# Performance work log

Hardware: AMD Instinct MI355X
Metric: run time of the kernel (lower is better)

The kernel has to match this reference:

```python
import jax, jax.numpy as jnp
import numpy as np

N, M, E = 100000, 500, 300000
XS, GS, OUT, HEADS = 100, 100, 100, 2
SLOPE = 0.2
EPS = 1e-12


def l2norm(x, axis):
    n = jnp.linalg.norm(x, axis=axis, keepdims=True)
    return x / jnp.maximum(n, EPS)


def gat_layer(h_ijk, ends, n, W, att):
    # W: [heads*out, in_dim] (no bias); att: [1, heads, out]
    heads, out = att.shape[1], att.shape[2]
    c = (h_ijk @ W.T).reshape(-1, heads, out)               # [E, H, D]
    a = jnp.sum(att * c, axis=2, keepdims=True)             # [E, H, 1]
    e = jnp.exp(-jax.nn.leaky_relu(a, SLOPE))
    denom = jax.ops.segment_sum(e, ends, num_segments=n)    # [n, H, 1]
    alpha = e / denom[ends]                                 # segment softmax (dropout=eval/identity)
    h = jax.ops.segment_sum(alpha * c, ends, num_segments=n)  # [n, H, D]
    h = jax.nn.elu(h)
    h = l2norm(h, axis=2)
    return h.reshape(n, heads * out)


def merge_layer(h_in, h_out, Wi, bi, Wo, bo, Wl, bl):
    hi = h_in @ Wi.T + bi
    ho = h_out @ Wo.T + bo
    lam = jax.nn.sigmoid(jnp.concatenate([hi, ho], axis=1) @ Wl.T + bl)
    h = lam * hi + (1.0 - lam) * ho
    return l2norm(jax.nn.elu(h), axis=1)


def setup_inputs() -> dict:
    key = jax.random.key(0)
    ks = jax.random.split(key, 24)
    D = HEADS * OUT  # 200
    in1 = 2 * XS + GS   # 300
    in2 = 3 * D         # 600
    s = 0.05
    return {
        'edge_idx': jax.random.randint(ks[0], (2, E), 0, N),
        'edge_type': jax.random.randint(ks[1], (E,), 0, M),
        'path_idx': jax.random.randint(ks[2], (2, 8), 0, N),
        'path_type': jax.random.randint(ks[3], (2, 8), 0, M),
        'use_path': 0,
        'x': jax.random.normal(ks[4], (N, XS), jnp.float32),
        'g': jax.random.normal(ks[5], (M, GS), jnp.float32),
        'W_in1': s * jax.random.normal(ks[6], (D, in1), jnp.float32),
        'att_in1': s * jax.random.normal(ks[7], (1, HEADS, OUT), jnp.float32),
        'W_out1': s * jax.random.normal(ks[8], (D, in1), jnp.float32),
        'att_out1': s * jax.random.normal(ks[9], (1, HEADS, OUT), jnp.float32),
        'Wi1': s * jax.random.normal(ks[10], (D, D), jnp.float32), 'bi1': jnp.zeros((D,), jnp.float32),
        'Wo1': s * jax.random.normal(ks[11], (D, D), jnp.float32), 'bo1': jnp.zeros((D,), jnp.float32),
        'Wl1': s * jax.random.normal(ks[12], (1, 2 * D), jnp.float32), 'bl1': jnp.zeros((1,), jnp.float32),
        'Wr': s * jax.random.normal(ks[13], (D, GS), jnp.float32), 'br': jnp.zeros((D,), jnp.float32),
        'Wf': s * jax.random.normal(ks[14], (D, in1), jnp.float32), 'bf': jnp.zeros((D,), jnp.float32),
        'W_in2': s * jax.random.normal(ks[15], (D, in2), jnp.float32),
        'att_in2': s * jax.random.normal(ks[16], (1, 1, D), jnp.float32),
        'W_out2': s * jax.random.normal(ks[17], (D, in2), jnp.float32),
        'att_out2': s * jax.random.normal(ks[18], (1, 1, D), jnp.float32),
        'Wi2': s * jax.random.normal(ks[19], (D, D), jnp.float32), 'bi2': jnp.zeros((D,), jnp.float32),
        'Wo2': s * jax.random.normal(ks[20], (D, D), jnp.float32), 'bo2': jnp.zeros((D,), jnp.float32),
        'Wl2': s * jax.random.normal(ks[21], (1, 2 * D), jnp.float32), 'bl2': jnp.zeros((1,), jnp.float32),
        'W_ent': s * jax.random.normal(ks[22], (D, XS), jnp.float32),
    }


def reference(edge_idx, edge_type, path_idx, path_type, use_path, x, g,
              W_in1, att_in1, W_out1, att_out1, Wi1, bi1, Wo1, bo1, Wl1, bl1,
              Wr, br, Wf, bf,
              W_in2, att_in2, W_out2, att_out2, Wi2, bi2, Wo2, bo2, Wl2, bl2,
              W_ent):
    n, m = x.shape[0], g.shape[0]
    x = l2norm(x, axis=1)  # x_initial is renormalized each forward
    row, col = edge_idx[0], edge_idx[1]
    # hop 1: gather-concat per-edge features [E, 2*XS+GS]
    h_ijk = jnp.concatenate([x[row], x[col], g[edge_type]], axis=1)
    h_in = gat_layer(h_ijk, col, n, W_in1, att_in1)
    h_out = gat_layer(h_ijk, row, n, W_out1, att_out1)
    h = merge_layer(h_in, h_out, Wi1, bi1, Wo1, bo1, Wl1, bl1)
    # relation layer
    g_edges = jax.ops.segment_sum(h_ijk, edge_type, num_segments=m)
    g_edges = jax.nn.elu(l2norm(g_edges, axis=1))
    g_prime = (g @ Wr.T + br) + (g_edges @ Wf.T + bf)
    # hop 2
    h_ijk2 = jnp.concatenate([h[row], h[col], g_prime[edge_type]], axis=1)
    h_in2 = gat_layer(h_ijk2, col, n, W_in2, att_in2)
    h_out2 = gat_layer(h_ijk2, row, n, W_out2, att_out2)
    h = merge_layer(h_in2, h_out2, Wi2, bi2, Wo2, bo2, Wl2, bl2)
    # entity residual layer
    h_prime = x @ W_ent.T + h
    return h_prime
```

## Files before the change

### kernel.cpp

```cpp
#include <hip/hip_runtime.h>
#include <cstddef>
#include <cstdint>

#define WSLOPE 0.2f
#define WEPS 1e-12f

typedef __attribute__((ext_vector_type(8))) short bf16x8;
typedef __attribute__((ext_vector_type(4))) float f32x4;

__device__ __forceinline__ float waveSum(float v) {
#pragma unroll
    for (int off = 32; off > 0; off >>= 1) v += __shfl_xor(v, off, 64);
    return v;
}
__device__ __forceinline__ float eluf(float v) { return v > 0.f ? v : expm1f(v); }
__device__ __forceinline__ short f2bf(float f) {
    union { float f; uint32_t u; } v; v.f = f;
    uint32_t r = v.u + 0x7FFF + ((v.u >> 16) & 1);
    return (short)(r >> 16);
}

__global__ void k_invnorm(const float* __restrict__ x, float* __restrict__ invn, int N) {
    int wid = blockIdx.x * 4 + (threadIdx.x >> 6);
    int lane = threadIdx.x & 63;
    if (wid >= N) return;
    const float* p = x + (size_t)wid * 100;
    float a = p[lane];
    float ss = a * a;
    if (lane < 36) { float b = p[lane + 64]; ss += b * b; }
    ss = waveSum(ss);
    if (lane == 0) invn[wid] = 1.f / fmaxf(sqrtf(ss), WEPS);
}

__global__ void k_count(const int* __restrict__ keys, int* __restrict__ cnt, int n) {
    int i = blockIdx.x * 256 + threadIdx.x;
    if (i < n) atomicAdd(&cnt[keys[i]], 1);
}

#define SCAN_CHUNK 2048
__global__ void k_blocksum(const int* __restrict__ cnt, int* __restrict__ bsum, int n) {
    __shared__ int sh[256];
    int b = blockIdx.x, t = threadIdx.x;
    int base = b * SCAN_CHUNK;
    int s = 0;
    for (int i = t; i < SCAN_CHUNK; i += 256) { int idx = base + i; if (idx < n) s += cnt[idx]; }
    sh[t] = s; __syncthreads();
    for (int off = 128; off > 0; off >>= 1) { if (t < off) sh[t] += sh[t + off]; __syncthreads(); }
    if (t == 0) bsum[b] = sh[0];
}

__global__ void k_scanwrite(const int* __restrict__ cnt, const int* __restrict__ bsum,
                            int* __restrict__ offs, int* __restrict__ cur, int n, int nb) {
    __shared__ int sh[256];
    __shared__ int sbase;
    int b = blockIdx.x, t = threadIdx.x;
    if (t == 0) { int s = 0; for (int i = 0; i < b; ++i) s += bsum[i]; sbase = s; }
    __syncthreads();
    int base = b * SCAN_CHUNK;
    int loc[8]; int ts = 0;
#pragma unroll
    for (int i = 0; i < 8; ++i) { int idx = base + t * 8 + i; int v = (idx < n) ? cnt[idx] : 0; loc[i] = ts; ts += v; }
    sh[t] = ts; __syncthreads();
    for (int off = 1; off < 256; off <<= 1) {
        int v = (t >= off) ? sh[t - off] : 0;
        __syncthreads();
        sh[t] += v;
        __syncthreads();
    }
    int excl = (t == 0) ? 0 : sh[t - 1];
    int gbase = sbase + excl;
#pragma unroll
    for (int i = 0; i < 8; ++i) {
        int idx = base + t * 8 + i;
        if (idx < n) { offs[idx] = gbase + loc[i]; cur[idx] = gbase + loc[i]; }
    }
    if (b == nb - 1 && t == 255) offs[n] = sbase + sh[255];
}

__global__ void k_scatter(const int* __restrict__ keys, int* __restrict__ cur, int* __restrict__ lists, int n) {
    int i = blockIdx.x * 256 + threadIdx.x;
    if (i < n) { int p = atomicAdd(&cur[keys[i]], 1); lists[p] = i; }
}

__global__ void k_watt(const float* __restrict__ att, const float* __restrict__ W,
                       float* __restrict__ wa, int H, int DH, int K) {
    int id = blockIdx.x * 256 + threadIdx.x;
    if (id >= H * K) return;
    int h = id / K, k = id % K;
    float s = 0.f;
    for (int j = 0; j < DH; ++j) s += att[h * DH + j] * W[(size_t)(h * DH + j) * K + k];
    wa[id] = s;
}

template<bool HOP2>
__global__ void k_dots(const float* __restrict__ feat, const float* __restrict__ invn,
                       const float* __restrict__ wa, float* __restrict__ rdot,
                       float* __restrict__ cdot, int N) {
    int wid = blockIdx.x * 4 + (threadIdx.x >> 6);
    int lane = threadIdx.x & 63;
    if (wid >= N) return;
    if (!HOP2) {
        float inv = invn[wid];
        const float* p = feat + (size_t)wid * 100;
        float f0 = p[lane] * inv;
        float f1 = (lane < 36) ? p[lane + 64] * inv : 0.f;
#pragma unroll
        for (int h = 0; h < 2; ++h) {
            const float* w = wa + h * 300;
            float r = f0 * w[lane] + ((lane < 36) ? f1 * w[lane + 64] : 0.f);
            float c = f0 * w[100 + lane] + ((lane < 36) ? f1 * w[100 + lane + 64] : 0.f);
            r = waveSum(r); c = waveSum(c);
            if (lane == 0) { rdot[wid * 2 + h] = r; cdot[wid * 2 + h] = c; }
        }
    } else {
        const float* p = feat + (size_t)wid * 200;
        float r = 0.f, c = 0.f;
#pragma unroll
        for (int m = 0; m < 4; ++m) {
            int d = lane + m * 64;
            if (d < 200) { float f = p[d]; r += f * wa[d]; c += f * wa[200 + d]; }
        }
        r = waveSum(r); c = waveSum(c);
        if (lane == 0) { rdot[wid] = r; cdot[wid] = c; }
    }
}

__global__ void k_gdot(const float* __restrict__ gsrc, const float* __restrict__ wa,
                       float* __restrict__ gdot, int M, int H, int GL, int K) {
    int id = blockIdx.x * 256 + threadIdx.x;
    if (id >= M * H) return;
    int m = id / H, h = id % H;
    float s = 0.f;
    const float* w = wa + h * K + 2 * GL;
    const float* gm = gsrc + (size_t)m * GL;
    for (int kk = 0; kk < GL; ++kk) s += gm[kk] * w[kk];
    gdot[id] = s;
}

__global__ void k_projg(const float* __restrict__ gsrc, const float* __restrict__ W,
                        float* __restrict__ pg, int M, int GL, int K) {
    int id = blockIdx.x * 256 + threadIdx.x;
    if (id >= M * 200) return;
    int m = id / 200, d = id % 200;
    float s = 0.f;
    const float* gm = gsrc + (size_t)m * GL;
    const float* w = W + (size_t)d * K + 2 * GL;
    for (int kk = 0; kk < GL; ++kk) s += gm[kk] * w[kk];
    pg[id] = s;
}

__global__ void k_ew(const int* __restrict__ row, const int* __restrict__ col, const int* __restrict__ et,
                     const float* __restrict__ rdot, const float* __restrict__ cdot,
                     const float* __restrict__ gdot, float* __restrict__ ew, int E, int H) {
    int id = blockIdx.x * 256 + threadIdx.x;
    if (id >= E * H) return;
    int e = id / H, h = id - e * H;
    float a = rdot[row[e] * H + h] + cdot[col[e] * H + h] + gdot[et[e] * H + h];
    float lr = a > 0.f ? a : WSLOPE * a;
    ew[id] = expf(-lr);
}

template<int H, bool HOP2>
__global__ void k_agg(const int* __restrict__ offs, const int* __restrict__ lists,
                      const int* __restrict__ nbrArr, const int* __restrict__ etype,
                      const float* __restrict__ ew, const float* __restrict__ projg,
                      const float* __restrict__ feat, const float* __restrict__ invn,
                      short* __restrict__ agg_b, float* __restrict__ hb, int n0, int n1) {
    int node = n0 + blockIdx.x * 4 + (threadIdx.x >> 6);
    int lane = threadIdx.x & 63;
    if (node >= n1) return;
    int o = offs[node];
    int deg = offs[node + 1] - o;
    float va[7];
#pragma unroll
    for (int m = 0; m < 7; ++m) va[m] = 0.f;
    if (deg > 0) {
        float s0 = 0.f, s1 = 0.f;
        for (int i = lane; i < deg; i += 64) {
            int e = lists[o + i];
            s0 += ew[e * H];
            if (H == 2) s1 += ew[e * H + 1];
        }
        s0 = waveSum(s0);
        float rd0 = 1.f / s0, rd1 = rd0;
        if (H == 2) { s1 = waveSum(s1); rd1 = 1.f / s1; }
        for (int j = 0; j < deg; ++j) {
            int e = lists[o + j];
            float a0 = ew[e * H] * rd0;
            float a1 = (H == 2) ? ew[e * H + 1] * rd1 : a0;
            int nbr = nbrArr[e];
            int et = etype[e];
            const float* pgr = projg + (size_t)et * 200;
            if (!HOP2) {
                float inv = invn[nbr];
                const float* fr = feat + (size_t)nbr * 100;
#pragma unroll
                for (int m = 0; m < 7; ++m) {
                    int d = lane + m * 64;
                    if (d < 200) {
                        int kk = d >= 100 ? d - 100 : d;
                        float al = d < 100 ? a0 : a1;
                        va[m] += al * fr[kk] * inv;
                    } else if (d < 400) {
                        int dd = d - 200;
                        float al = dd < 100 ? a0 : a1;
                        va[m] += al * pgr[dd];
                    }
                }
            } else {
                const float* fr = feat + (size_t)nbr * 200;
#pragma unroll
                for (int m = 0; m < 7; ++m) {
                    int d = lane + m * 64;
                    if (d < 200) va[m] += a0 * fr[d];
                    else if (d < 400) va[m] += a0 * pgr[d - 200];
                }
            }
        }
    }
    size_t rb = (size_t)(node - n0);
#pragma unroll
    for (int m = 0; m < 7; ++m) {
        int d = lane + m * 64;
        if (d < 200) {
            int slot = HOP2 ? d : (d < 100 ? d : d + 12);
            agg_b[rb * 224 + slot] = f2bf(va[m]);
        } else if (d < 400) {
            hb[rb * 200 + (d - 200)] = va[m];
        }
    }
    if (!HOP2) {
        if (lane < 24) { int s = lane < 12 ? 100 + lane : 200 + lane; agg_b[rb * 224 + s] = 0; }
    } else {
        if (lane < 24) agg_b[rb * 224 + 200 + lane] = 0;
    }
}

template<int KSTEPS, bool BIAS, bool ACC, bool DEGMASK>
__launch_bounds__(256)
__global__ void k_mgemm(const short* __restrict__ A, const short* __restrict__ Wb,
                        const float* __restrict__ bias, const int* __restrict__ degoffs,
                        float* __restrict__ out, int rows) {
    constexpr int LDA = KSTEPS * 32;
    const int t = threadIdx.x;
    const int wv = t >> 6, l = t & 63;
    const int lhi = l >> 4, llo = l & 15;
    const int rbase = blockIdx.x * 64 + wv * 16;
    f32x4 acc[13];
#pragma unroll
    for (int j = 0; j < 13; ++j) acc[j] = f32x4{0.f, 0.f, 0.f, 0.f};
    const short* arow = A + (size_t)(rbase + llo) * LDA + lhi * 8;
#pragma unroll
    for (int kt = 0; kt < KSTEPS; ++kt) {
        bf16x8 a = *(const bf16x8*)(arow + kt * 32);
#pragma unroll
        for (int j = 0; j < 13; ++j) {
            bf16x8 b = *(const bf16x8*)(Wb + (size_t)(j * 16 + llo) * LDA + kt * 32 + lhi * 8);
            acc[j] = __builtin_amdgcn_mfma_f32_16x16x32_bf16(a, b, acc[j], 0, 0, 0);
        }
    }
    const int r0 = rbase + lhi * 4;
#pragma unroll
    for (int e = 0; e < 4; ++e) {
        int r = r0 + e;
        if (r >= rows) continue;
        float dm = 1.f;
        if (DEGMASK) dm = (degoffs[r + 1] - degoffs[r] == 0) ? 0.f : 1.f;
        float* orow = out + (size_t)r * 200;
#pragma unroll
        for (int j = 0; j < 13; ++j) {
            int d = j * 16 + llo;
            if (d < 200) {
                float v = acc[j][e] * dm;
                if (BIAS) v += bias[d];
                if (ACC) v += orow[d];
                orow[d] = v;
            }
        }
    }
}

__global__ void k_prepw(const float* __restrict__ W, int ldW, int koff, int Klen, int Kpad,
                        int mode, short* __restrict__ Wb) {
    int id = blockIdx.x * 256 + threadIdx.x;
    int tot = 208 * Kpad;
    if (id >= tot) return;
    int d = id / Kpad, k = id - d * Kpad;
    float v = 0.f;
    if (d < 200) {
        if (mode == 0) { if (k < Klen) v = W[(size_t)d * ldW + koff + k]; }
        else { int h = d / 100; int kk = k - h * 112; if (kk >= 0 && kk < 100) v = W[(size_t)d * ldW + koff + kk]; }
    }
    Wb[id] = f2bf(v);
}

__global__ void k_xcb(const float* __restrict__ x, const float* __restrict__ invn,
                      short* __restrict__ sb, int rows) {
    int id = blockIdx.x * 256 + threadIdx.x;
    if (id >= rows * 128) return;
    int r = id >> 7, k = id & 127;
    sb[id] = f2bf(k < 100 ? x[(size_t)r * 100 + k] * invn[r] : 0.f);
}

__global__ void k_h1b(const float* __restrict__ h1, short* __restrict__ sb, int rows) {
    int id = blockIdx.x * 256 + threadIdx.x;
    if (id >= rows * 224) return;
    int r = id / 224, k = id - r * 224;
    sb[id] = f2bf(k < 200 ? h1[(size_t)r * 200 + k] : 0.f);
}

template<int DH, int H>
__global__ void gat_post2(const float* __restrict__ hb, short* __restrict__ pb, int rowsH) {
    int nh = blockIdx.x * 4 + (threadIdx.x >> 6);
    int lane = threadIdx.x & 63;
    if (nh >= rowsH) return;
    const float* p = hb + (size_t)nh * DH;
    constexpr int MM = (DH + 63) / 64;
    float v[MM];
    float ss = 0.f;
#pragma unroll
    for (int m = 0; m < MM; ++m) {
        int d = lane + m * 64;
        v[m] = 0.f;
        if (d < DH) { v[m] = eluf(p[d]); ss += v[m] * v[m]; }
    }
    ss = waveSum(ss);
    float inv = 1.f / fmaxf(sqrtf(ss), WEPS);
    short* ob = pb + (size_t)(nh / H) * 224 + (size_t)(nh % H) * DH;
#pragma unroll
    for (int m = 0; m < MM; ++m) {
        int d = lane + m * 64;
        if (d < DH) ob[d] = f2bf(v[m] * inv);
    }
}

__global__ void merge_comb(const float* __restrict__ hi, const float* __restrict__ ho,
                           const float* __restrict__ Wl, const float* __restrict__ bl,
                           float* __restrict__ out, int N) {
    int wid = blockIdx.x * 4 + (threadIdx.x >> 6);
    int lane = threadIdx.x & 63;
    if (wid >= N) return;
    float vi[4], vo[4];
    float s = 0.f;
#pragma unroll
    for (int m = 0; m < 4; ++m) {
        int d = lane + m * 64;
        vi[m] = 0.f; vo[m] = 0.f;
        if (d < 200) {
            vi[m] = hi[(size_t)wid * 200 + d];
            vo[m] = ho[(size_t)wid * 200 + d];
            s += Wl[d] * vi[m] + Wl[200 + d] * vo[m];
        }
    }
    s = waveSum(s);
    float lam = 1.f / (1.f + expf(-(s + bl[0])));
    float hv[4];
    float ss = 0.f;
#pragma unroll
    for (int m = 0; m < 4; ++m) {
        int d = lane + m * 64;
        hv[m] = 0.f;
        if (d < 200) {
            float h = lam * vi[m] + (1.f - lam) * vo[m];
            hv[m] = eluf(h);
            ss += hv[m] * hv[m];
        }
    }
    ss = waveSum(ss);
    float inv = 1.f / fmaxf(sqrtf(ss), WEPS);
#pragma unroll
    for (int m = 0; m < 4; ++m) {
        int d = lane + m * 64;
        if (d < 200) out[(size_t)wid * 200 + d] = hv[m] * inv;
    }
}

__global__ void k_gedges(const int* __restrict__ eidx, const int* __restrict__ lists,
                         const int* __restrict__ offs,
                         const float* __restrict__ x, const float* __restrict__ invn,
                         const float* __restrict__ g, float* __restrict__ ge_n, int E) {
    __shared__ float red[5];
    __shared__ float stot;
    int m = blockIdx.x, t = threadIdx.x;
    int o = offs[m];
    int n = offs[m + 1] - o;
    float acc = 0.f;
    if (t < 200) {
        for (int i = 0; i < n; ++i) {
            int e = lists[o + i];
            if (t < 100) { int r = eidx[e];     acc += x[(size_t)r * 100 + t] * invn[r]; }
            else         { int r = eidx[E + e]; acc += x[(size_t)r * 100 + t - 100] * invn[r]; }
        }
    } else if (t < 300) {
        acc = (float)n * g[(size_t)m * 100 + (t - 200)];
    }
    float sq = (t < 300) ? acc * acc : 0.f;
    sq = waveSum(sq);
    if ((t & 63) == 0) red[t >> 6] = sq;
    __syncthreads();
    if (t == 0) {
        float s2 = 0.f;
        for (int i = 0; i < 5; ++i) s2 += red[i];
        stot = 1.f / fmaxf(sqrtf(s2), WEPS);
    }
    __syncthreads();
    if (t < 300) ge_n[(size_t)m * 300 + t] = eluf(acc * stot);
}

__global__ void k_gprime(const float* __restrict__ g, const float* __restrict__ ge_n,
                         const float* __restrict__ Wr, const float* __restrict__ br,
                         const float* __restrict__ Wf, const float* __restrict__ bf,
                         float* __restrict__ gp, int M) {
    int m = blockIdx.x, d = threadIdx.x;
    if (d >= 200) return;
    float s = br[d] + bf[d];
    const float* gm = g + (size_t)m * 100;
    const float* gem = ge_n + (size_t)m * 300;
    const float* wr = Wr + (size_t)d * 100;
    const float* wf = Wf + (size_t)d * 300;
    for (int k = 0; k < 100; ++k) s += wr[k] * gm[k];
    for (int k = 0; k < 300; ++k) s += wf[k] * gem[k];
    gp[(size_t)m * 200 + d] = s;
}

extern "C" void kernel_launch(void* const* d_in, const int* in_sizes, int n_in,
                              void* d_out, int out_size, void* d_ws, size_t ws_size,
                              hipStream_t stream) {
    const int* eidx   = (const int*)d_in[0];
    const int* etype  = (const int*)d_in[1];
    const float* x    = (const float*)d_in[5];
    const float* g    = (const float*)d_in[6];
    const float* W_in1  = (const float*)d_in[7];
    const float* att_in1 = (const float*)d_in[8];
    const float* W_out1 = (const float*)d_in[9];
    const float* att_out1 = (const float*)d_in[10];
    const float* Wi1 = (const float*)d_in[11]; const float* bi1 = (const float*)d_in[12];
    const float* Wo1 = (const float*)d_in[13]; const float* bo1 = (const float*)d_in[14];
    const float* Wl1 = (const float*)d_in[15]; const float* bl1 = (const float*)d_in[16];
    const float* Wr  = (const float*)d_in[17]; const float* br  = (const float*)d_in[18];
    const float* Wf  = (const float*)d_in[19]; const float* bf  = (const float*)d_in[20];
    const float* W_in2  = (const float*)d_in[21]; const float* att_in2 = (const float*)d_in[22];
    const float* W_out2 = (const float*)d_in[23]; const float* att_out2 = (const float*)d_in[24];
    const float* Wi2 = (const float*)d_in[25]; const float* bi2 = (const float*)d_in[26];
    const float* Wo2 = (const float*)d_in[27]; const float* bo2 = (const float*)d_in[28];
    const float* Wl2 = (const float*)d_in[29]; const float* bl2 = (const float*)d_in[30];
    const float* W_ent = (const float*)d_in[31];

    const int E = in_sizes[1];
    const int N = in_sizes[5] / 100;
    const int M = in_sizes[6] / 100;
    float* out = (float*)d_out;
    const int* row = eidx;
    const int* col = eidx + E;

    char* w = (char*)d_ws;
    size_t off_b = 0;
    auto alloc = [&](size_t bytes) -> void* {
        void* p = w + off_b;
        off_b += (bytes + 255) & ~(size_t)255;
        return p;
    };
    float* invn  = (float*)alloc((size_t)N * 4);
    float* h1    = (float*)alloc((size_t)N * 200 * 4);
    int* offs_in = (int*)alloc((size_t)(N + 1) * 4);
    int* lists_in= (int*)alloc((size_t)E * 4);
    int* offs_out= (int*)alloc((size_t)(N + 1) * 4);
    int* lists_out=(int*)alloc((size_t)E * 4);
    int* offsT   = (int*)alloc((size_t)(M + 1) * 4);
    int* listsT  = (int*)alloc((size_t)E * 4);
    int* cnt     = (int*)alloc((size_t)N * 4);
    int* cur     = (int*)alloc((size_t)N * 4);
    int* bsum    = (int*)alloc((size_t)64 * 4);
    float* wa_in = (float*)alloc((size_t)1200 * 4);
    float* wa_out= (float*)alloc((size_t)1200 * 4);
    float* rdot_in = (float*)alloc((size_t)N * 2 * 4);
    float* cdot_in = (float*)alloc((size_t)N * 2 * 4);
    float* rdot_out= (float*)alloc((size_t)N * 2 * 4);
    float* cdot_out= (float*)alloc((size_t)N * 2 * 4);
    float* gdot_in = (float*)alloc((size_t)M * 2 * 4);
    float* gdot_out= (float*)alloc((size_t)M * 2 * 4);
    float* ew_in   = (float*)alloc((size_t)E * 2 * 4);
    float* ew_out  = (float*)alloc((size_t)E * 2 * 4);
    float* pg_in   = (float*)alloc((size_t)M * 200 * 4);
    float* pg_out  = (float*)alloc((size_t)M * 200 * 4);
    float* ge_n    = (float*)alloc((size_t)M * 300 * 4);
    float* gp      = (float*)alloc((size_t)M * 200 * 4);
    short* Ws_in1  = (short*)alloc((size_t)208 * 128 * 2);
    short* Ws_out1 = (short*)alloc((size_t)208 * 128 * 2);
    short* Wa_in1  = (short*)alloc((size_t)208 * 224 * 2);
    short* Wa_out1 = (short*)alloc((size_t)208 * 224 * 2);
    short* Wm_i1   = (short*)alloc((size_t)208 * 224 * 2);
    short* Wm_o1   = (short*)alloc((size_t)208 * 224 * 2);
    short* Ws_in2  = (short*)alloc((size_t)208 * 224 * 2);
    short* Ws_out2 = (short*)alloc((size_t)208 * 224 * 2);
    short* Wa_in2  = (short*)alloc((size_t)208 * 224 * 2);
    short* Wa_out2 = (short*)alloc((size_t)208 * 224 * 2);
    short* Wm_i2   = (short*)alloc((size_t)208 * 224 * 2);
    short* Wm_o2   = (short*)alloc((size_t)208 * 224 * 2);
    short* Wb_ent  = (short*)alloc((size_t)208 * 128 * 2);

    if (off_b >= ws_size) return;
    size_t rem = ws_size - off_b;
    long long Cll = (long long)(rem / 3072);
    long long Nr64 = ((long long)N + 63) & ~63LL;
    int C = (int)(Cll > Nr64 ? Nr64 : Cll);
    C &= ~63;
    if (C < 64) return;
    float* hbA   = (float*)alloc((size_t)C * 200 * 4);
    float* hbB   = (float*)alloc((size_t)C * 200 * 4);
    short* agg_b = (short*)alloc((size_t)C * 224 * 2);
    short* post_b= (short*)alloc((size_t)C * 224 * 2);
    short* sb    = (short*)alloc((size_t)C * 224 * 2);
    if (off_b > ws_size) return;

    const int gE = (E + 255) / 256;
    const int gN4 = (N + 3) / 4;

    k_invnorm<<<gN4, 256, 0, stream>>>(x, invn, N);

    hipMemsetAsync(post_b, 0, (size_t)C * 224 * 2, stream);

    const int gW224 = (208 * 224 + 255) / 256;
    const int gW128 = (208 * 128 + 255) / 256;
    k_prepw<<<gW128, 256, 0, stream>>>(W_in1, 300, 100, 100, 128, 0, Ws_in1);
    k_prepw<<<gW128, 256, 0, stream>>>(W_out1, 300, 0, 100, 128, 0, Ws_out1);
    k_prepw<<<gW224, 256, 0, stream>>>(W_in1, 300, 0, 100, 224, 1, Wa_in1);
    k_prepw<<<gW224, 256, 0, stream>>>(W_out1, 300, 100, 100, 224, 1, Wa_out1);
    k_prepw<<<gW224, 256, 0, stream>>>(Wi1, 200, 0, 200, 224, 0, Wm_i1);
    k_prepw<<<gW224, 256, 0, stream>>>(Wo1, 200, 0, 200, 224, 0, Wm_o1);
    k_prepw<<<gW224, 256, 0, stream>>>(W_in2, 600, 200, 200, 224, 0, Ws_in2);
    k_prepw<<<gW224, 256, 0, stream>>>(W_out2, 600, 0, 200, 224, 0, Ws_out2);
    k_prepw<<<gW224, 256, 0, stream>>>(W_in2, 600, 0, 200, 224, 0, Wa_in2);
    k_prepw<<<gW224, 256, 0, stream>>>(W_out2, 600, 200, 200, 224, 0, Wa_out2);
    k_prepw<<<gW224, 256, 0, stream>>>(Wi2, 200, 0, 200, 224, 0, Wm_i2);
    k_prepw<<<gW224, 256, 0, stream>>>(Wo2, 200, 0, 200, 224, 0, Wm_o2);
    k_prepw<<<gW128, 256, 0, stream>>>(W_ent, 100, 0, 100, 128, 0, Wb_ent);

    int nbN = (N + SCAN_CHUNK - 1) / SCAN_CHUNK;
    int nbM = (M + SCAN_CHUNK - 1) / SCAN_CHUNK;
    hipMemsetAsync(cnt, 0, (size_t)N * 4, stream);
    k_count<<<gE, 256, 0, stream>>>(col, cnt, E);
    k_blocksum<<<nbN, 256, 0, stream>>>(cnt, bsum, N);
    k_scanwrite<<<nbN, 256, 0, stream>>>(cnt, bsum, offs_in, cur, N, nbN);
    k_scatter<<<gE, 256, 0, stream>>>(col, cur, lists_in, E);

    hipMemsetAsync(cnt, 0, (size_t)N * 4, stream);
    k_count<<<gE, 256, 0, stream>>>(row, cnt, E);
    k_blocksum<<<nbN, 256, 0, stream>>>(cnt, bsum, N);
    k_scanwrite<<<nbN, 256, 0, stream>>>(cnt, bsum, offs_out, cur, N, nbN);
    k_scatter<<<gE, 256, 0, stream>>>(row, cur, lists_out, E);

    hipMemsetAsync(cnt, 0, (size_t)M * 4, stream);
    k_count<<<gE, 256, 0, stream>>>(etype, cnt, E);
    k_blocksum<<<nbM, 256, 0, stream>>>(cnt, bsum, M);
    k_scanwrite<<<nbM, 256, 0, stream>>>(cnt, bsum, offsT, cur, M, nbM);
    k_scatter<<<gE, 256, 0, stream>>>(etype, cur, listsT, E);

    k_watt<<<(2 * 300 + 255) / 256, 256, 0, stream>>>(att_in1, W_in1, wa_in, 2, 100, 300);
    k_watt<<<(2 * 300 + 255) / 256, 256, 0, stream>>>(att_out1, W_out1, wa_out, 2, 100, 300);
    k_dots<false><<<gN4, 256, 0, stream>>>(x, invn, wa_in, rdot_in, cdot_in, N);
    k_dots<false><<<gN4, 256, 0, stream>>>(x, invn, wa_out, rdot_out, cdot_out, N);
    k_gdot<<<(M * 2 + 255) / 256, 256, 0, stream>>>(g, wa_in, gdot_in, M, 2, 100, 300);
    k_gdot<<<(M * 2 + 255) / 256, 256, 0, stream>>>(g, wa_out, gdot_out, M, 2, 100, 300);
    k_projg<<<(M * 200 + 255) / 256, 256, 0, stream>>>(g, W_in1, pg_in, M, 100, 300);
    k_projg<<<(M * 200 + 255) / 256, 256, 0, stream>>>(g, W_out1, pg_out, M, 100, 300);
    k_ew<<<(E * 2 + 255) / 256, 256, 0, stream>>>(row, col, etype, rdot_in, cdot_in, gdot_in, ew_in, E, 2);
    k_ew<<<(E * 2 + 255) / 256, 256, 0, stream>>>(row, col, etype, rdot_out, cdot_out, gdot_out, ew_out, E, 2);

    for (int n0 = 0; n0 < N; n0 += C) {
        int rows = (N - n0 < C) ? (N - n0) : C;
        int n1 = n0 + rows;
        int ga = (rows + 3) / 4;
        int gb = (rows + 63) / 64;
        k_xcb<<<(rows * 128 + 255) / 256, 256, 0, stream>>>(x + (size_t)n0 * 100, invn + n0, sb, rows);
        k_agg<2, false><<<ga, 256, 0, stream>>>(offs_in, lists_in, row, etype, ew_in, pg_in, x, invn, agg_b, hbA, n0, n1);
        k_mgemm<4, false, true, true><<<gb, 256, 0, stream>>>(sb, Ws_in1, nullptr, offs_in + n0, hbA, rows);
        k_mgemm<7, false, true, false><<<gb, 256, 0, stream>>>(agg_b, Wa_in1, nullptr, nullptr, hbA, rows);
        k_agg<2, false><<<ga, 256, 0, stream>>>(offs_out, lists_out, col, etype, ew_out, pg_out, x, invn, agg_b, hbB, n0, n1);
        k_mgemm<4, false, true, true><<<gb, 256, 0, stream>>>(sb, Ws_out1, nullptr, offs_out + n0, hbB, rows);
        k_mgemm<7, false, true, false><<<gb, 256, 0, stream>>>(agg_b, Wa_out1, nullptr, nullptr, hbB, rows);
        gat_post2<100, 2><<<(2 * rows + 3) / 4, 256, 0, stream>>>(hbA, post_b, 2 * rows);
        k_mgemm<7, true, false, false><<<gb, 256, 0, stream>>>(post_b, Wm_i1, bi1, nullptr, hbA, rows);
        gat_post2<100, 2><<<(2 * rows + 3) / 4, 256, 0, stream>>>(hbB, post_b, 2 * rows);
        k_mgemm<7, true, false, false><<<gb, 256, 0, stream>>>(post_b, Wm_o1, bo1, nullptr, hbB, rows);
        merge_comb<<<ga, 256, 0, stream>>>(hbA, hbB, Wl1, bl1, h1 + (size_t)n0 * 200, rows);
    }

    k_gedges<<<M, 320, 0, stream>>>(eidx, listsT, offsT, x, invn, g, ge_n, E);
    k_gprime<<<M, 256, 0, stream>>>(g, ge_n, Wr, br, Wf, bf, gp, M);

    k_watt<<<(600 + 255) / 256, 256, 0, stream>>>(att_in2, W_in2, wa_in, 1, 200, 600);
    k_watt<<<(600 + 255) / 256, 256, 0, stream>>>(att_out2, W_out2, wa_out, 1, 200, 600);
    k_dots<true><<<gN4, 256, 0, stream>>>(h1, nullptr, wa_in, rdot_in, cdot_in, N);
    k_dots<true><<<gN4, 256, 0, stream>>>(h1, nullptr, wa_out, rdot_out, cdot_out, N);
    k_gdot<<<(M + 255) / 256, 256, 0, stream>>>(gp, wa_in, gdot_in, M, 1, 200, 600);
    k_gdot<<<(M + 255) / 256, 256, 0, stream>>>(gp, wa_out, gdot_out, M, 1, 200, 600);
    k_projg<<<(M * 200 + 255) / 256, 256, 0, stream>>>(gp, W_in2, pg_in, M, 200, 600);
    k_projg<<<(M * 200 + 255) / 256, 256, 0, stream>>>(gp, W_out2, pg_out, M, 200, 600);
    k_ew<<<(E + 255) / 256, 256, 0, stream>>>(row, col, etype, rdot_in, cdot_in, gdot_in, ew_in, E, 1);
    k_ew<<<(E + 255) / 256, 256, 0, stream>>>(row, col, etype, rdot_out, cdot_out, gdot_out, ew_out, E, 1);

    for (int n0 = 0; n0 < N; n0 += C) {
        int rows = (N - n0 < C) ? (N - n0) : C;
        int n1 = n0 + rows;
        int ga = (rows + 3) / 4;
        int gb = (rows + 63) / 64;
        k_h1b<<<(rows * 224 + 255) / 256, 256, 0, stream>>>(h1 + (size_t)n0 * 200, sb, rows);
        k_agg<1, true><<<ga, 256, 0, stream>>>(offs_in, lists_in, row, etype, ew_in, pg_in, h1, nullptr, agg_b, hbA, n0, n1);
        k_mgemm<7, false, true, true><<<gb, 256, 0, stream>>>(sb, Ws_in2, nullptr, offs_in + n0, hbA, rows);
        k_mgemm<7, false, true, false><<<gb, 256, 0, stream>>>(agg_b, Wa_in2, nullptr, nullptr, hbA, rows);
        k_agg<1, true><<<ga, 256, 0, stream>>>(offs_out, lists_out, col, etype, ew_out, pg_out, h1, nullptr, agg_b, hbB, n0, n1);
        k_mgemm<7, false, true, true><<<gb, 256, 0, stream>>>(sb, Ws_out2, nullptr, offs_out + n0, hbB, rows);
        k_mgemm<7, false, true, false><<<gb, 256, 0, stream>>>(agg_b, Wa_out2, nullptr, nullptr, hbB, rows);
        gat_post2<200, 1><<<ga, 256, 0, stream>>>(hbA, post_b, rows);
        k_mgemm<7, true, false, false><<<gb, 256, 0, stream>>>(post_b, Wm_i2, bi2, nullptr, hbA, rows);
        gat_post2<200, 1><<<ga, 256, 0, stream>>>(hbB, post_b, rows);
        k_mgemm<7, true, false, false><<<gb, 256, 0, stream>>>(post_b, Wm_o2, bo2, nullptr, hbB, rows);
        merge_comb<<<ga, 256, 0, stream>>>(hbA, hbB, Wl2, bl2, out + (size_t)n0 * 200, rows);
        k_xcb<<<(rows * 128 + 255) / 256, 256, 0, stream>>>(x + (size_t)n0 * 100, invn + n0, sb, rows);
        k_mgemm<4, false, true, false><<<gb, 256, 0, stream>>>(sb, Wb_ent, nullptr, nullptr, out + (size_t)n0 * 200, rows);
    }
}
```

Measured before the change: 3.055 ms.

## Move relation-layer and per-type projections onto bf16 MFMA GEMMs

Replaces the scalar per-type projection kernels (k_projg) and the relation layer's g' computation (k_gprime) with the existing MFMA GEMM kernel, which now takes a runtime lda. The relation-edge aggregation becomes one wave per type and writes bf16 output straight into a combined [g | g_edges] buffer, so a single GEMM with fused Wr/Wf weights and a merged bias can produce g'. This removes the scalar FP32 dot-product loops and the 500-block launch with serial inner loops. In exchange these paths now compute in bf16, which lowers precision, and several extra weight-prep launches are added.

```diff
diff --git a/kernel.cpp b/kernel.cpp
--- a/kernel.cpp
+++ b/kernel.cpp
@@ -135,18 +135,6 @@
     const float* gm = gsrc + (size_t)m * GL;
     for (int kk = 0; kk < GL; ++kk) s += gm[kk] * w[kk];
     gdot[id] = s;
-}
-
-__global__ void k_projg(const float* __restrict__ gsrc, const float* __restrict__ W,
-                        float* __restrict__ pg, int M, int GL, int K) {
-    int id = blockIdx.x * 256 + threadIdx.x;
-    if (id >= M * 200) return;
-    int m = id / 200, d = id % 200;
-    float s = 0.f;
-    const float* gm = gsrc + (size_t)m * GL;
-    const float* w = W + (size_t)d * K + 2 * GL;
-    for (int kk = 0; kk < GL; ++kk) s += gm[kk] * w[kk];
-    pg[id] = s;
 }
 
 __global__ void k_ew(const int* __restrict__ row, const int* __restrict__ col, const int* __restrict__ et,
@@ -240,8 +228,8 @@
 __launch_bounds__(256)
 __global__ void k_mgemm(const short* __restrict__ A, const short* __restrict__ Wb,
                         const float* __restrict__ bias, const int* __restrict__ degoffs,
-                        float* __restrict__ out, int rows) {
-    constexpr int LDA = KSTEPS * 32;
+                        float* __restrict__ out, int rows, int lda) {
+    constexpr int LDW = KSTEPS * 32;
     const int t = threadIdx.x;
     const int wv = t >> 6, l = t & 63;
     const int lhi = l >> 4, llo = l & 15;
@@ -249,13 +237,13 @@
     f32x4 acc[13];
 #pragma unroll
     for (int j = 0; j < 13; ++j) acc[j] = f32x4{0.f, 0.f, 0.f, 0.f};
-    const short* arow = A + (size_t)(rbase + llo) * LDA + lhi * 8;
+    const short* arow = A + (size_t)(rbase + llo) * lda + lhi * 8;
 #pragma unroll
     for (int kt = 0; kt < KSTEPS; ++kt) {
         bf16x8 a = *(const bf16x8*)(arow + kt * 32);
 #pragma unroll
         for (int j = 0; j < 13; ++j) {
-            bf16x8 b = *(const bf16x8*)(Wb + (size_t)(j * 16 + llo) * LDA + kt * 32 + lhi * 8);
+            bf16x8 b = *(const bf16x8*)(Wb + (size_t)(j * 16 + llo) * LDW + kt * 32 + lhi * 8);
             acc[j] = __builtin_amdgcn_mfma_f32_16x16x32_bf16(a, b, acc[j], 0, 0, 0);
         }
     }
@@ -294,12 +282,38 @@
     Wb[id] = f2bf(v);
 }
 
+__global__ void k_prepwrf(const float* __restrict__ Wr, const float* __restrict__ Wf,
+                          short* __restrict__ Wb) {
+    int id = blockIdx.x * 256 + threadIdx.x;
+    if (id >= 208 * 448) return;
+    int d = id / 448, k = id - d * 448;
+    float v = 0.f;
+    if (d < 200) {
+        if (k < 100) v = Wr[(size_t)d * 100 + k];
+        else if (k >= 128 && k < 428) v = Wf[(size_t)d * 300 + (k - 128)];
+    }
+    Wb[id] = f2bf(v);
+}
+
+__global__ void k_brf(const float* __restrict__ br, const float* __restrict__ bf,
+                      float* __restrict__ brf) {
+    int d = threadIdx.x;
+    if (d < 200) brf[d] = br[d] + bf[d];
+}
+
 __global__ void k_xcb(const float* __restrict__ x, const float* __restrict__ invn,
                       short* __restrict__ sb, int rows) {
     int id = blockIdx.x * 256 + threadIdx.x;
     if (id >= rows * 128) return;
     int r = id >> 7, k = id & 127;
     sb[id] = f2bf(k < 100 ? x[(size_t)r * 100 + k] * invn[r] : 0.f);
+}
+
+__global__ void k_gcb(const float* __restrict__ g, short* __restrict__ gb, int rows) {
+    int id = blockIdx.x * 256 + threadIdx.x;
+    if (id >= rows * 128) return;
+    int r = id >> 7, k = id & 127;
+    gb[(size_t)r * 448 + k] = f2bf(k < 100 ? g[(size_t)r * 100 + k] : 0.f);
 }
 
 __global__ void k_h1b(const float* __restrict__ h1, short* __restrict__ sb, int rows) {
@@ -375,52 +389,48 @@
     }
 }
 
-__global__ void k_gedges(const int* __restrict__ eidx, const int* __restrict__ lists,
-                         const int* __restrict__ offs,
-                         const float* __restrict__ x, const float* __restrict__ invn,
-                         const float* __restrict__ g, float* __restrict__ ge_n, int E) {
-    __shared__ float red[5];
-    __shared__ float stot;
-    int m = blockIdx.x, t = threadIdx.x;
-    int o = offs[m];
-    int n = offs[m + 1] - o;
-    float acc = 0.f;
-    if (t < 200) {
-        for (int i = 0; i < n; ++i) {
-            int e = lists[o + i];
-            if (t < 100) { int r = eidx[e];     acc += x[(size_t)r * 100 + t] * invn[r]; }
-            else         { int r = eidx[E + e]; acc += x[(size_t)r * 100 + t - 100] * invn[r]; }
-        }
-    } else if (t < 300) {
-        acc = (float)n * g[(size_t)m * 100 + (t - 200)];
-    }
-    float sq = (t < 300) ? acc * acc : 0.f;
-    sq = waveSum(sq);
-    if ((t & 63) == 0) red[t >> 6] = sq;
-    __syncthreads();
-    if (t == 0) {
-        float s2 = 0.f;
-        for (int i = 0; i < 5; ++i) s2 += red[i];
-        stot = 1.f / fmaxf(sqrtf(s2), WEPS);
-    }
-    __syncthreads();
-    if (t < 300) ge_n[(size_t)m * 300 + t] = eluf(acc * stot);
-}
-
-__global__ void k_gprime(const float* __restrict__ g, const float* __restrict__ ge_n,
-                         const float* __restrict__ Wr, const float* __restrict__ br,
-                         const float* __restrict__ Wf, const float* __restrict__ bf,
-                         float* __restrict__ gp, int M) {
-    int m = blockIdx.x, d = threadIdx.x;
-    if (d >= 200) return;
-    float s = br[d] + bf[d];
-    const float* gm = g + (size_t)m * 100;
-    const float* gem = ge_n + (size_t)m * 300;
-    const float* wr = Wr + (size_t)d * 100;
-    const float* wf = Wf + (size_t)d * 300;
-    for (int k = 0; k < 100; ++k) s += wr[k] * gm[k];
-    for (int k = 0; k < 300; ++k) s += wf[k] * gem[k];
-    gp[(size_t)m * 200 + d] = s;
+__global__ void k_gedges_w(const int* __restrict__ eidx, const int* __restrict__ listsT,
+                           const int* __restrict__ offsT,
+                           const float* __restrict__ x, const float* __restrict__ invn,
+                           const float* __restrict__ g, short* __restrict__ gcomb,
+                           int M, int E) {
+    int m = blockIdx.x * 4 + (threadIdx.x >> 6);
+    int lane = threadIdx.x & 63;
+    if (m >= M) return;
+    int o = offsT[m];
+    int deg = offsT[m + 1] - o;
+    float acc[5];
+#pragma unroll
+    for (int j = 0; j < 5; ++j) acc[j] = 0.f;
+    for (int i = 0; i < deg; ++i) {
+        int e = listsT[o + i];
+        int r = eidx[e];
+        int c = eidx[E + e];
+        float ir = invn[r], ic = invn[c];
+#pragma unroll
+        for (int j = 0; j < 4; ++j) {
+            int d = lane + j * 64;
+            if (d < 100) acc[j] += x[(size_t)r * 100 + d] * ir;
+            else if (d < 200) acc[j] += x[(size_t)c * 100 + d - 100] * ic;
+        }
+    }
+#pragma unroll
+    for (int j = 3; j < 5; ++j) {
+        int d = lane + j * 64;
+        if (d >= 200 && d < 300) acc[j] = (float)deg * g[(size_t)m * 100 + (d - 200)];
+    }
+    float ss = 0.f;
+#pragma unroll
+    for (int j = 0; j < 5; ++j) ss += acc[j] * acc[j];
+    ss = waveSum(ss);
+    float inv = 1.f / fmaxf(sqrtf(ss), WEPS);
+    short* orow = gcomb + (size_t)m * 448 + 128;
+#pragma unroll
+    for (int j = 0; j < 5; ++j) {
+        int d = lane + j * 64;
+        if (d < 300) orow[d] = f2bf(eluf(acc[j] * inv));
+        else if (d < 320) orow[d] = 0;
+    }
 }
 
 extern "C" void kernel_launch(void* const* d_in, const int* in_sizes, int n_in,
@@ -449,6 +459,7 @@
     const int E = in_sizes[1];
     const int N = in_sizes[5] / 100;
     const int M = in_sizes[6] / 100;
+    const int Mr = (M + 63) & ~63;
     float* out = (float*)d_out;
     const int* row = eidx;
     const int* col = eidx + E;
@@ -483,8 +494,8 @@
     float* ew_out  = (float*)alloc((size_t)E * 2 * 4);
     float* pg_in   = (float*)alloc((size_t)M * 200 * 4);
     float* pg_out  = (float*)alloc((size_t)M * 200 * 4);
-    float* ge_n    = (float*)alloc((size_t)M * 300 * 4);
     float* gp      = (float*)alloc((size_t)M * 200 * 4);
+    short* gcomb   = (short*)alloc((size_t)Mr * 448 * 2);
     short* Ws_in1  = (short*)alloc((size_t)208 * 128 * 2);
     short* Ws_out1 = (short*)alloc((size_t)208 * 128 * 2);
     short* Wa_in1  = (short*)alloc((size_t)208 * 224 * 2);
@@ -498,6 +509,12 @@
     short* Wm_i2   = (short*)alloc((size_t)208 * 224 * 2);
     short* Wm_o2   = (short*)alloc((size_t)208 * 224 * 2);
     short* Wb_ent  = (short*)alloc((size_t)208 * 128 * 2);
+    short* Wg_in1  = (short*)alloc((size_t)208 * 128 * 2);
+    short* Wg_out1 = (short*)alloc((size_t)208 * 128 * 2);
+    short* Wg_in2  = (short*)alloc((size_t)208 * 224 * 2);
+    short* Wg_out2 = (short*)alloc((size_t)208 * 224 * 2);
+    short* Wrf_b   = (short*)alloc((size_t)208 * 448 * 2);
+    float* brf     = (float*)alloc((size_t)200 * 4);
 
     if (off_b >= ws_size) return;
     size_t rem = ws_size - off_b;
@@ -515,6 +532,8 @@
 
     const int gE = (E + 255) / 256;
     const int gN4 = (N + 3) / 4;
+    const int gM64 = (M + 63) / 64;
+    const int gM4 = (M + 3) / 4;
 
     k_invnorm<<<gN4, 256, 0, stream>>>(x, invn, N);
 
@@ -522,6 +541,7 @@
 
     const int gW224 = (208 * 224 + 255) / 256;
     const int gW128 = (208 * 128 + 255) / 256;
+    const int gW448 = (208 * 448 + 255) / 256;
     k_prepw<<<gW128, 256, 0, stream>>>(W_in1, 300, 100, 100, 128, 0, Ws_in1);
     k_prepw<<<gW128, 256, 0, stream>>>(W_out1, 300, 0, 100, 128, 0, Ws_out1);
     k_prepw<<<gW224, 256, 0, stream>>>(W_in1, 300, 0, 100, 224, 1, Wa_in1);
@@ -535,6 +555,12 @@
     k_prepw<<<gW224, 256, 0, stream>>>(Wi2, 200, 0, 200, 224, 0, Wm_i2);
     k_prepw<<<gW224, 256, 0, stream>>>(Wo2, 200, 0, 200, 224, 0, Wm_o2);
     k_prepw<<<gW128, 256, 0, stream>>>(W_ent, 100, 0, 100, 128, 0, Wb_ent);
+    k_prepw<<<gW128, 256, 0, stream>>>(W_in1, 300, 200, 100, 128, 0, Wg_in1);
+    k_prepw<<<gW128, 256, 0, stream>>>(W_out1, 300, 200, 100, 128, 0, Wg_out1);
+    k_prepw<<<gW224, 256, 0, stream>>>(W_in2, 600, 400, 200, 224, 0, Wg_in2);
+    k_prepw<<<gW224, 256, 0, stream>>>(W_out2, 600, 400, 200, 224, 0, Wg_out2);
+    k_prepwrf<<<gW448, 256, 0, stream>>>(Wr, Wf, Wrf_b);
+    k_brf<<<1, 256, 0, stream>>>(br, bf, brf);
 
     int nbN = (N + SCAN_CHUNK - 1) / SCAN_CHUNK;
     int nbM = (M + SCAN_CHUNK - 1) / SCAN_CHUNK;
@@ -562,8 +588,9 @@
     k_dots<false><<<gN4, 256, 0, stream>>>(x, invn, wa_out, rdot_out, cdot_out, N);
     k_gdot<<<(M * 2 + 255) / 256, 256, 0, stream>>>(g, wa_in, gdot_in, M, 2, 100, 300);
     k_gdot<<<(M * 2 + 255) / 256, 256, 0, stream>>>(g, wa_out, gdot_out, M, 2, 100, 300);
-    k_projg<<<(M * 200 + 255) / 256, 256, 0, stream>>>(g, W_in1, pg_in, M, 100, 300);
-    k_projg<<<(M * 200 + 255) / 256, 256, 0, stream>>>(g, W_out1, pg_out, M, 100, 300);
+    k_gcb<<<((int)(((size_t)M * 128 + 255) / 256)), 256, 0, stream>>>(g, gcomb, M);
+    k_mgemm<4, false, false, false><<<gM64, 256, 0, stream>>>(gcomb, Wg_in1, nullptr, nullptr, pg_in, M, 448);
+    k_mgemm<4, false, false, false><<<gM64, 256, 0, stream>>>(gcomb, Wg_out1, nullptr, nullptr, pg_out, M, 448);
     k_ew<<<(E * 2 + 255) / 256, 256, 0, stream>>>(row, col, etype, rdot_in, cdot_in, gdot_in, ew_in, E, 2);
     k_ew<<<(E * 2 + 255) / 256, 256, 0, stream>>>(row, col, etype, rdot_out, cdot_out, gdot_out, ew_out, E, 2);
 
@@ -574,20 +601,20 @@
         int gb = (rows + 63) / 64;
         k_xcb<<<(rows * 128 + 255) / 256, 256, 0, stream>>>(x + (size_t)n0 * 100, invn + n0, sb, rows);
         k_agg<2, false><<<ga, 256, 0, stream>>>(offs_in, lists_in, row, etype, ew_in, pg_in, x, invn, agg_b, hbA, n0, n1);
-        k_mgemm<4, false, true, true><<<gb, 256, 0, stream>>>(sb, Ws_in1, nullptr, offs_in + n0, hbA, rows);
-        k_mgemm<7, false, true, false><<<gb, 256, 0, stream>>>(agg_b, Wa_in1, nullptr, nullptr, hbA, rows);
+        k_mgemm<4, false, true, true><<<gb, 256, 0, stream>>>(sb, Ws_in1, nullptr, offs_in + n0, hbA, rows, 128);
+        k_mgemm<7, false, true, false><<<gb, 256, 0, stream>>>(agg_b, Wa_in1, nullptr, nullptr, hbA, rows, 224);
         k_agg<2, false><<<ga, 256, 0, stream>>>(offs_out, lists_out, col, etype, ew_out, pg_out, x, invn, agg_b, hbB, n0, n1);
-        k_mgemm<4, false, true, true><<<gb, 256, 0, stream>>>(sb, Ws_out1, nullptr, offs_out + n0, hbB, rows);
-        k_mgemm<7, false, true, false><<<gb, 256, 0, stream>>>(agg_b, Wa_out1, nullptr, nullptr, hbB, rows);
+        k_mgemm<4, false, true, true><<<gb, 256, 0, stream>>>(sb, Ws_out1, nullptr, offs_out + n0, hbB, rows, 128);
+        k_mgemm<7, false, true, false><<<gb, 256, 0, stream>>>(agg_b, Wa_out1, nullptr, nullptr, hbB, rows, 224);
         gat_post2<100, 2><<<(2 * rows + 3) / 4, 256, 0, stream>>>(hbA, post_b, 2 * rows);
-        k_mgemm<7, true, false, false><<<gb, 256, 0, stream>>>(post_b, Wm_i1, bi1, nullptr, hbA, rows);
+        k_mgemm<7, true, false, false><<<gb, 256, 0, stream>>>(post_b, Wm_i1, bi1, nullptr, hbA, rows, 224);
         gat_post2<100, 2><<<(2 * rows + 3) / 4, 256, 0, stream>>>(hbB, post_b, 2 * rows);
-        k_mgemm<7, true, false, false><<<gb, 256, 0, stream>>>(post_b, Wm_o1, bo1, nullptr, hbB, rows);
+        k_mgemm<7, true, false, false><<<gb, 256, 0, stream>>>(post_b, Wm_o1, bo1, nullptr, hbB, rows, 224);
         merge_comb<<<ga, 256, 0, stream>>>(hbA, hbB, Wl1, bl1, h1 + (size_t)n0 * 200, rows);
     }
 
-    k_gedges<<<M, 320, 0, stream>>>(eidx, listsT, offsT, x, invn, g, ge_n, E);
-    k_gprime<<<M, 256, 0, stream>>>(g, ge_n, Wr, br, Wf, bf, gp, M);
+    k_gedges_w<<<gM4, 256, 0, stream>>>(eidx, listsT, offsT, x, invn, g, gcomb, M, E);
+    k_mgemm<14, true, false, false><<<gM64, 256, 0, stream>>>(gcomb, Wrf_b, brf, nullptr, gp, M, 448);
 
     k_watt<<<(600 + 255) / 256, 256, 0, stream>>>(att_in2, W_in2, wa_in, 1, 200, 600);
     k_watt<<<(600 + 255) / 256, 256, 0, stream>>>(att_out2, W_out2, wa_out, 1, 200, 600);
@@ -595,8 +622,9 @@
     k_dots<true><<<gN4, 256, 0, stream>>>(h1, nullptr, wa_out, rdot_out, cdot_out, N);
     k_gdot<<<(M + 255) / 256, 256, 0, stream>>>(gp, wa_in, gdot_in, M, 1, 200, 600);
     k_gdot<<<(M + 255) / 256, 256, 0, stream>>>(gp, wa_out, gdot_out, M, 1, 200, 600);
-    k_projg<<<(M * 200 + 255) / 256, 256, 0, stream>>>(gp, W_in2, pg_in, M, 200, 600);
-    k_projg<<<(M * 200 + 255) / 256, 256, 0, stream>>>(gp, W_out2, pg_out, M, 200, 600);
+    k_h1b<<<((int)(((size_t)M * 224 + 255) / 256)), 256, 0, stream>>>(gp, gcomb, M);
+    k_mgemm<7, false, false, false><<<gM64, 256, 0, stream>>>(gcomb, Wg_in2, nullptr, nullptr, pg_in, M, 224);
+    k_mgemm<7, false, false, false><<<gM64, 256, 0, stream>>>(gcomb, Wg_out2, nullptr, nullptr, pg_out, M, 224);
     k_ew<<<(E + 255) / 256, 256, 0, stream>>>(row, col, etype, rdot_in, cdot_in, gdot_in, ew_in, E, 1);
     k_ew<<<(E + 255) / 256, 256, 0, stream>>>(row, col, etype, rdot_out, cdot_out, gdot_out, ew_out, E, 1);
 
@@ -607,17 +635,17 @@
         int gb = (rows + 63) / 64;
         k_h1b<<<(rows * 224 + 255) / 256, 256, 0, stream>>>(h1 + (size_t)n0 * 200, sb, rows);
         k_agg<1, true><<<ga, 256, 0, stream>>>(offs_in, lists_in, row, etype, ew_in, pg_in, h1, nullptr, agg_b, hbA, n0, n1);
-        k_mgemm<7, false, true, true><<<gb, 256, 0, stream>>>(sb, Ws_in2, nullptr, offs_in + n0, hbA, rows);
-        k_mgemm<7, false, true, false><<<gb, 256, 0, stream>>>(agg_b, Wa_in2, nullptr, nullptr, hbA, rows);
+        k_mgemm<7, false, true, true><<<gb, 256, 0, stream>>>(sb, Ws_in2, nullptr, offs_in + n0, hbA, rows, 224);
+        k_mgemm<7, false, true, false><<<gb, 256, 0, stream>>>(agg_b, Wa_in2, nullptr, nullptr, hbA, rows, 224);
         k_agg<1, true><<<ga, 256, 0, stream>>>(offs_out, lists_out, col, etype, ew_out, pg_out, h1, nullptr, agg_b, hbB, n0, n1);
-        k_mgemm<7, false, true, true><<<gb, 256, 0, stream>>>(sb, Ws_out2, nullptr, offs_out + n0, hbB, rows);
-        k_mgemm<7, false, true, false><<<gb, 256, 0, stream>>>(agg_b, Wa_out2, nullptr, nullptr, hbB, rows);
+        k_mgemm<7, false, true, true><<<gb, 256, 0, stream>>>(sb, Ws_out2, nullptr, offs_out + n0, hbB, rows, 224);
+        k_mgemm<7, false, true, false><<<gb, 256, 0, stream>>>(agg_b, Wa_out2, nullptr, nullptr, hbB, rows, 224);
         gat_post2<200, 1><<<ga, 256, 0, stream>>>(hbA, post_b, rows);
-        k_mgemm<7, true, false, false><<<gb, 256, 0, stream>>>(post_b, Wm_i2, bi2, nullptr, hbA, rows);
+        k_mgemm<7, true, false, false><<<gb, 256, 0, stream>>>(post_b, Wm_i2, bi2, nullptr, hbA, rows, 224);
         gat_post2<200, 1><<<ga, 256, 0, stream>>>(hbB, post_b, rows);
-        k_mgemm<7, true, false, false><<<gb, 256, 0, stream>>>(post_b, Wm_o2, bo2, nullptr, hbB, rows);
+        k_mgemm<7, true, false, false><<<gb, 256, 0, stream>>>(post_b, Wm_o2, bo2, nullptr, hbB, rows, 224);
         merge_comb<<<ga, 256, 0, stream>>>(hbA, hbB, Wl2, bl2, out + (size_t)n0 * 200, rows);
         k_xcb<<<(rows * 128 + 255) / 256, 256, 0, stream>>>(x + (size_t)n0 * 100, invn + n0, sb, rows);
-        k_mgemm<4, false, true, false><<<gb, 256, 0, stream>>>(sb, Wb_ent, nullptr, nullptr, out + (size_t)n0 * 200, rows);
-    }
-}
+        k_mgemm<4, false, true, false><<<gb, 256, 0, stream>>>(sb, Wb_ent, nullptr, nullptr, out + (size_t)n0 * 200, rows, 128);
+    }
+}
```

New measurement: 3.612 ms. +18.2%, slower.
